# Kernel tuning notes

Measured on AMD Instinct MI355X. Metric: run time of the kernel, lower is better.

Reference implementation:

```python
import jax, jax.numpy as jnp
import numpy as np

B, T, D, DFF, H, W = 2, 2048, 1024, 4096, 16, 512
HD = D // H
EPS = 1e-6
NEG = jnp.float32(-1e30)


def _rms(x, w):
    return x * jax.lax.rsqrt(jnp.mean(x * x, axis=-1, keepdims=True) + EPS) * w


def setup_inputs() -> dict:
    key = jax.random.key(0)
    ks = jax.random.split(key, 12)
    g = lambda k, shape, std: jax.random.normal(k, shape, jnp.float32) * std
    return {
        "x": jax.random.normal(ks[0], (B, T, D), jnp.float32),
        "retrieval_context": jax.random.normal(ks[1], (B, D), jnp.float32),
        "norm1_w": jnp.ones((D,), jnp.float32),
        "qkv_w": g(ks[2], (3 * D, D), 0.02),
        "qkv_b": jnp.zeros((3 * D,), jnp.float32),
        "proj_w": g(ks[3], (D, D), 0.02),
        "proj_b": jnp.zeros((D,), jnp.float32),
        "gate_w": g(ks[4], (3, D), 0.01),
        "gate_b": jnp.zeros((3,), jnp.float32),
        "ret_w": g(ks[5], (D, D), 0.01),
        "norm2_w": jnp.ones((D,), jnp.float32),
        "ffn_gate_w": g(ks[6], (DFF, D), 0.02),
        "ffn_up_w": g(ks[7], (DFF, D), 0.02),
        "ffn_down_w": g(ks[8], (D, DFF), 0.02),
    }


def reference(x, retrieval_context, norm1_w, qkv_w, qkv_b, proj_w, proj_b,
              gate_w, gate_b, ret_w, norm2_w, ffn_gate_w, ffn_up_w, ffn_down_w):
    # pre-norm
    h = _rms(x, norm1_w)  # (B,T,D)
    # qkv projection, split into heads
    qkv = h @ qkv_w.T + qkv_b  # (B,T,3D)
    q, k, v = jnp.split(qkv, 3, axis=-1)
    to_heads = lambda t: t.reshape(B, T, H, HD).transpose(0, 2, 1, 3)  # (B,H,T,HD)
    q, k, v = to_heads(q), to_heads(k), to_heads(v)
    # sliding-window causal mask: attend to j in [i-W+1, i]
    idx = jnp.arange(T)
    win = (idx[:, None] >= idx[None, :]) & (idx[:, None] - idx[None, :] < W)  # (T,T)
    scores = jnp.einsum("bhqd,bhkd->bhqk", q, k) / np.sqrt(HD).astype(np.float32)
    scores = jnp.where(win, scores, NEG)
    attn = jax.nn.softmax(scores, axis=-1)
    attn_out = jnp.einsum("bhqk,bhkd->bhqd", attn, v)  # (B,H,T,HD)
    attn_out = attn_out.transpose(0, 2, 1, 3).reshape(B, T, D)
    attn_out = attn_out @ proj_w.T + proj_b
    # retrieval stream (TRN disabled -> zeros, gate channel 1 hard-masked)
    ret_out = (retrieval_context @ ret_w.T)[:, None, :]  # (B,1,D) broadcast over T
    gate_logits = h @ gate_w.T + gate_b  # (B,T,3)
    gate_logits = gate_logits.at[:, :, 1].set(-1e9)  # enable_trn=False
    gates = jax.nn.softmax(gate_logits, axis=-1)
    mixed = gates[:, :, 0:1] * attn_out + gates[:, :, 2:3] * ret_out
    x = x + mixed
    # SwiGLU FFN
    h2 = _rms(x, norm2_w)
    ffn = (jax.nn.silu(h2 @ ffn_gate_w.T) * (h2 @ ffn_up_w.T)) @ ffn_down_w.T
    return x + ffn
```

## Files before the change

kernel.cpp:

```cpp
#include <hip/hip_runtime.h>
#include <hip/hip_bf16.h>

typedef __bf16 bf16_t;
typedef __bf16 bf16x8 __attribute__((ext_vector_type(8)));
typedef __bf16 bf16x4v __attribute__((ext_vector_type(4)));
typedef float f32x4 __attribute__((ext_vector_type(4)));

static constexpr int Bn = 2, Tn = 2048, Dn = 1024, DFFn = 4096, Hn = 16, HDn = 64, Wn = 512;
static constexpr int Mn = Bn * Tn;

#define MFMA16(a, b, c) __builtin_amdgcn_mfma_f32_16x16x32_bf16(a, b, c, 0, 0, 0)

typedef __attribute__((address_space(3))) void lds_void;
typedef const __attribute__((address_space(1))) void gbl_void;

__global__ __launch_bounds__(256) void cvt_f32_bf16_kernel(const float4* __restrict__ src,
                                                           bf16x4v* __restrict__ dst, int n4) {
  int i = blockIdx.x * 256 + threadIdx.x;
  if (i < n4) {
    float4 v = src[i];
    bf16x4v o;
    o[0] = (bf16_t)v.x; o[1] = (bf16_t)v.y; o[2] = (bf16_t)v.z; o[3] = (bf16_t)v.w;
    dst[i] = o;
  }
}

__device__ __forceinline__ float blockReduceSum(float v, float* sbuf) {
#pragma unroll
  for (int off = 32; off > 0; off >>= 1) v += __shfl_down(v, off, 64);
  int lane = threadIdx.x & 63, wid = threadIdx.x >> 6;
  __syncthreads();
  if (lane == 0) sbuf[wid] = v;
  __syncthreads();
  return sbuf[0] + sbuf[1] + sbuf[2] + sbuf[3];
}

template <bool GATE>
__global__ __launch_bounds__(256) void rmsnorm_kernel(const float* __restrict__ x,
                                                      const float* __restrict__ w,
                                                      bf16_t* __restrict__ out,
                                                      const float* __restrict__ gw,
                                                      const float* __restrict__ gb,
                                                      float* __restrict__ gates) {
  __shared__ float sbuf[4];
  int row = blockIdx.x, tid = threadIdx.x;
  const float4* xr = (const float4*)(x + (long)row * Dn);
  float4 v = xr[tid];
  float ss = v.x * v.x + v.y * v.y + v.z * v.z + v.w * v.w;
  ss = blockReduceSum(ss, sbuf);
  float rms = rsqrtf(ss * (1.0f / Dn) + 1e-6f);
  float4 wv = ((const float4*)w)[tid];
  float h0 = v.x * rms * wv.x, h1 = v.y * rms * wv.y;
  float h2 = v.z * rms * wv.z, h3 = v.w * rms * wv.w;
  bf16x4v o;
  o[0] = (bf16_t)h0; o[1] = (bf16_t)h1; o[2] = (bf16_t)h2; o[3] = (bf16_t)h3;
  ((bf16x4v*)(out + (long)row * Dn))[tid] = o;
  if (GATE) {
    float4 g0v = ((const float4*)gw)[tid];
    float4 g2v = ((const float4*)(gw + 2 * Dn))[tid];
    float l0 = h0 * g0v.x + h1 * g0v.y + h2 * g0v.z + h3 * g0v.w;
    float l2 = h0 * g2v.x + h1 * g2v.y + h2 * g2v.z + h3 * g2v.w;
    l0 = blockReduceSum(l0, sbuf);
    l2 = blockReduceSum(l2, sbuf);
    if (tid == 0) {
      l0 += gb[0];
      l2 += gb[2];
      float mx = fmaxf(l0, l2);
      float e0 = __expf(l0 - mx), e2 = __expf(l2 - mx);
      float inv = 1.0f / (e0 + e2);
      gates[2 * row] = e0 * inv;
      gates[2 * row + 1] = e2 * inv;
    }
  }
}

__global__ __launch_bounds__(512, 2) void gemm256_kernel(const bf16_t* __restrict__ Ag,
                                                         const bf16_t* __restrict__ Wt, int K,
                                                         int N, const float* __restrict__ bias,
                                                         bf16_t* __restrict__ outb) {
  __shared__ bf16_t lds2[65536];
  const int tid = threadIdx.x;
  const int wid = tid >> 6, lane = tid & 63;
  const int wr = wid >> 2, wc = wid & 3;
  const int m0 = blockIdx.y * 256, n0 = blockIdx.x * 256;
  const int lr = lane & 15, lg = lane >> 4;
  const int lterm = (lr * 32 + lg * 8) ^ (((lr >> 3) & 1) << 4);
  const int colsw = (lane & 3) * 8 ^ (((lane >> 5) & 1) << 4);
  const int NT = K >> 6;

  auto stageA = [&](int buf, int half, int t) {
#pragma unroll
    for (int q = 0; q < 2; q++) {
      int s = q * 8 + wid, s_r = s >> 1, s_c = s & 1;
      const bf16_t* src =
          Ag + (long)(m0 + half * 128 + s_r * 16 + (lane >> 2)) * K + (long)t * 64 + s_c * 32 + colsw;
      bf16_t* dst = &lds2[buf * 32768 + (half * 8 + s_r) * 1024 + s_c * 512];
      __builtin_amdgcn_global_load_lds((gbl_void*)src, (lds_void*)dst, 16, 0, 0);
    }
  };
  auto stageB = [&](int buf, int half, int t) {
#pragma unroll
    for (int q = 0; q < 2; q++) {
      int s = q * 8 + wid, s_r = s >> 1, s_c = s & 1;
      const bf16_t* src =
          Wt + (long)(n0 + half * 128 + s_r * 16 + (lane >> 2)) * K + (long)t * 64 + s_c * 32 + colsw;
      bf16_t* dst = &lds2[buf * 32768 + 16384 + (half * 8 + s_r) * 1024 + s_c * 512];
      __builtin_amdgcn_global_load_lds((gbl_void*)src, (lds_void*)dst, 16, 0, 0);
    }
  };

  f32x4 acc[8][4];
#pragma unroll
  for (int i = 0; i < 8; i++)
#pragma unroll
    for (int j = 0; j < 4; j++) acc[i][j] = (f32x4){0.f, 0.f, 0.f, 0.f};

  stageB(0, 0, 0);
  stageB(0, 1, 0);
  stageA(0, 0, 0);
  stageA(0, 1, 0);
  if (NT > 1) {
    stageB(1, 0, 1);
    stageB(1, 1, 1);
    asm volatile("s_waitcnt vmcnt(4)" ::: "memory");
  } else {
    asm volatile("s_waitcnt vmcnt(0)" ::: "memory");
  }
  __builtin_amdgcn_sched_barrier(0);
  __builtin_amdgcn_s_barrier();

#define LDA(mi, ks) (*(const bf16x8*)&lds2[ca + ((wr << 3) + (mi)) * 1024 + (ks)*512 + lterm])
#define LDB(ni, ks) (*(const bf16x8*)&lds2[cb + ((wc << 2) + (ni)) * 1024 + (ks)*512 + lterm])

#define GPHASE(mi0, ...)                                                                  \
  do {                                                                                    \
    bf16x8 a0k0 = LDA(mi0, 0), a0k1 = LDA(mi0, 1);                                        \
    bf16x8 a1k0 = LDA((mi0) + 1, 0), a1k1 = LDA((mi0) + 1, 1);                            \
    __VA_ARGS__;                                                                          \
    __builtin_amdgcn_s_barrier();                                                         \
    asm volatile("s_waitcnt lgkmcnt(0)" ::: "memory");                                    \
    __builtin_amdgcn_sched_barrier(0);                                                    \
    __builtin_amdgcn_s_setprio(1);                                                        \
    _Pragma("unroll") for (int ni = 0; ni < 4; ni++) {                                    \
      acc[mi0][ni] = MFMA16(a0k0, bfr[ni][0], acc[mi0][ni]);                              \
      acc[mi0][ni] = MFMA16(a0k1, bfr[ni][1], acc[mi0][ni]);                              \
      acc[(mi0) + 1][ni] = MFMA16(a1k0, bfr[ni][0], acc[(mi0) + 1][ni]);                  \
      acc[(mi0) + 1][ni] = MFMA16(a1k1, bfr[ni][1], acc[(mi0) + 1][ni]);                  \
    }                                                                                     \
    __builtin_amdgcn_s_setprio(0);                                                        \
    __builtin_amdgcn_s_barrier();                                                         \
  } while (0)

#define GTILE(t, cur)                                                                     \
  do {                                                                                    \
    const int ca = (cur)*32768, cb = ca + 16384;                                          \
    bf16x8 bfr[4][2];                                                                     \
    _Pragma("unroll") for (int ni = 0; ni < 4; ni++) {                                    \
      bfr[ni][0] = LDB(ni, 0);                                                            \
      bfr[ni][1] = LDB(ni, 1);                                                            \
    }                                                                                     \
    GPHASE(0, {                                                                           \
      if ((t) + 1 < NT) {                                                                 \
        stageA(1 - (cur), 0, (t) + 1);                                                    \
        stageA(1 - (cur), 1, (t) + 1);                                                    \
      }                                                                                   \
    });                                                                                   \
    GPHASE(2, {                                                                           \
      if ((t) + 2 < NT) stageB((cur), 0, (t) + 2);                                        \
    });                                                                                   \
    GPHASE(4, {                                                                           \
      if ((t) + 2 < NT) stageB((cur), 1, (t) + 2);                                        \
    });                                                                                   \
    GPHASE(6, {});                                                                        \
    if ((t) + 1 < NT) {                                                                   \
      if ((t) + 2 < NT)                                                                   \
        asm volatile("s_waitcnt vmcnt(4)" ::: "memory");                                  \
      else                                                                                \
        asm volatile("s_waitcnt vmcnt(0)" ::: "memory");                                  \
      __builtin_amdgcn_sched_barrier(0);                                                  \
      __builtin_amdgcn_s_barrier();                                                       \
    }                                                                                     \
  } while (0)

  for (int t = 0; t < NT; t += 2) {
    GTILE(t, 0);
    GTILE(t + 1, 1);
  }

#pragma unroll
  for (int mi = 0; mi < 8; mi++) {
#pragma unroll
    for (int rr = 0; rr < 4; rr++) {
      long r = m0 + wr * 128 + mi * 16 + lg * 4 + rr;
#pragma unroll
      for (int ni = 0; ni < 4; ni++) {
        int c = n0 + wc * 64 + ni * 16 + lr;
        float v = acc[mi][ni][rr];
        if (bias) v += bias[c];
        outb[r * N + c] = (bf16_t)v;
      }
    }
  }
#undef LDA
#undef LDB
#undef GPHASE
#undef GTILE
}

template <int EPI>
__global__ __launch_bounds__(256) void gemm_kernel(const bf16_t* __restrict__ A,
                                                   const bf16_t* __restrict__ Wt, int K, int N,
                                                   const float* __restrict__ bias,
                                                   bf16_t* __restrict__ outb,
                                                   float* __restrict__ outf,
                                                   const float* __restrict__ gates,
                                                   const float* __restrict__ ret,
                                                   const float* __restrict__ resid) {
  __shared__ bf16_t smem[8192];
  const int tid = threadIdx.x;
  const int w = tid >> 6, lane = tid & 63;
  const int wr = w >> 1, wc = w & 1;
  const int m0 = blockIdx.y * 128, n0 = blockIdx.x * 128;

  const bf16_t* gsrc[4];
#pragma unroll
  for (int q = 0; q < 4; q++) {
    int e = ((w * 4 + q) * 64 + lane) * 8;
    int rr = (e & 4095) >> 5, cc = e & 31;
    gsrc[q] = (e < 4096) ? (A + (long)(m0 + rr) * K + cc) : (Wt + (long)(n0 + rr) * K + cc);
  }
  bf16_t* lbase = &smem[(w * 4) * 512];

  f32x4 acc[4][4];
#pragma unroll
  for (int i = 0; i < 4; i++)
#pragma unroll
    for (int j = 0; j < 4; j++) acc[i][j] = (f32x4){0.f, 0.f, 0.f, 0.f};

  const int lr = lane & 15, lc = (lane >> 4) * 8;

  for (int kt = 0; kt < K; kt += 32) {
    if (kt) __syncthreads();
#pragma unroll
    for (int q = 0; q < 4; q++) {
      __builtin_amdgcn_global_load_lds((gbl_void*)(gsrc[q] + kt), (lds_void*)(lbase + q * 512), 16,
                                       0, 0);
    }
    __syncthreads();

    bf16x8 af[4], bfv[4];
#pragma unroll
    for (int i = 0; i < 4; i++) af[i] = *(const bf16x8*)&smem[(wr * 64 + i * 16 + lr) * 32 + lc];
#pragma unroll
    for (int i = 0; i < 4; i++)
      bfv[i] = *(const bf16x8*)&smem[4096 + (wc * 64 + i * 16 + lr) * 32 + lc];
#pragma unroll
    for (int mi = 0; mi < 4; mi++)
#pragma unroll
      for (int ni = 0; ni < 4; ni++) acc[mi][ni] = MFMA16(af[mi], bfv[ni], acc[mi][ni]);
  }

  const int lrow4 = (lane >> 4) * 4;
#pragma unroll
  for (int mi = 0; mi < 4; mi++) {
#pragma unroll
    for (int rr2 = 0; rr2 < 4; rr2++) {
      int r = m0 + wr * 64 + mi * 16 + lrow4 + rr2;
      float g0 = 0.f, g2 = 0.f;
      const float* retb = nullptr;
      if (EPI == 2) {
        g0 = gates[2 * r];
        g2 = gates[2 * r + 1];
        retb = ret + ((r >> 11) << 10);
      }
#pragma unroll
      for (int ni = 0; ni < 4; ni++) {
        int c = n0 + wc * 64 + ni * 16 + (lane & 15);
        float v = acc[mi][ni][rr2];
        long idx = (long)r * N + c;
        if (EPI == 0) {
          if (bias) v += bias[c];
          outb[idx] = (bf16_t)v;
        } else if (EPI == 2) {
          outf[idx] = resid[idx] + g0 * (v + bias[c]) + g2 * retb[c];
        } else {
          outf[idx] = resid[idx] + v;
        }
      }
    }
  }
}

__global__ __launch_bounds__(256) void retproj_kernel(const float* __restrict__ rc,
                                                      const float* __restrict__ rw,
                                                      float* __restrict__ out) {
  int gw = blockIdx.x * 4 + (threadIdx.x >> 6);
  int lane = threadIdx.x & 63;
  int b = gw >> 10, n = gw & 1023;
  float v = 0.f;
  for (int k = lane; k < Dn; k += 64) v += rc[b * Dn + k] * rw[(long)n * Dn + k];
#pragma unroll
  for (int off = 32; off > 0; off >>= 1) v += __shfl_down(v, off, 64);
  if (lane == 0) out[gw] = v;
}

__global__ __launch_bounds__(256) void attn_kernel(const bf16_t* __restrict__ qkv,
                                                   bf16_t* __restrict__ out) {
  __shared__ bf16_t psh[4][512];
  const int tid = threadIdx.x, w = tid >> 6, lane = tid & 63;
  const int qb = blockIdx.x, bh = blockIdx.y;
  const int b = bh >> 4, h = bh & 15;
  const int qw0 = qb * 64 + w * 16;
  const bf16_t* base = qkv + (long)b * Tn * 3072 + h * 64;
  const bf16_t* kb = base + Dn;
  const bf16_t* vb = base + 2 * Dn;
  const int lr = lane & 15, lg = lane >> 4;

  bf16x8 aq0 = *(const bf16x8*)(base + (long)(qw0 + lr) * 3072 + lg * 8);
  bf16x8 aq1 = *(const bf16x8*)(base + (long)(qw0 + lr) * 3072 + lg * 8 + 32);

  float m_run[4], l_run[4];
  f32x4 accv[4];
#pragma unroll
  for (int r = 0; r < 4; r++) { m_run[r] = -1e30f; l_run[r] = 0.f; }
#pragma unroll
  for (int c = 0; c < 4; c++) accv[c] = (f32x4){0.f, 0.f, 0.f, 0.f};

  int j_lo = qw0 - (Wn - 1);
  if (j_lo < 0) j_lo = 0;
  j_lo &= ~31;
  const int j_hi = qw0 + 15;

  for (int j0 = j_lo; j0 <= j_hi; j0 += 32) {
    f32x4 s[2];
#pragma unroll
    for (int hh = 0; hh < 2; hh++) {
      const bf16_t* kr = kb + (long)(j0 + hh * 16 + lr) * 3072 + lg * 8;
      bf16x8 k0 = *(const bf16x8*)kr;
      bf16x8 k1 = *(const bf16x8*)(kr + 32);
      f32x4 z = (f32x4){0.f, 0.f, 0.f, 0.f};
      z = MFMA16(aq0, k0, z);
      z = MFMA16(aq1, k1, z);
      s[hh] = z;
    }
    float mt[4];
#pragma unroll
    for (int r = 0; r < 4; r++) {
      int q = qw0 + lg * 4 + r;
      int c0 = j0 + lr, c1 = j0 + 16 + lr;
      float s0 = (q >= c0 && (q - c0) < Wn) ? s[0][r] * 0.125f : -1e30f;
      float s1 = (q >= c1 && (q - c1) < Wn) ? s[1][r] * 0.125f : -1e30f;
      s[0][r] = s0;
      s[1][r] = s1;
      mt[r] = fmaxf(s0, s1);
    }
#pragma unroll
    for (int off = 1; off < 16; off <<= 1)
#pragma unroll
      for (int r = 0; r < 4; r++) mt[r] = fmaxf(mt[r], __shfl_xor(mt[r], off, 64));
    float rs[4];
#pragma unroll
    for (int r = 0; r < 4; r++) {
      float nm = fmaxf(m_run[r], mt[r]);
      float alpha = __expf(m_run[r] - nm);
      m_run[r] = nm;
      float p0 = __expf(s[0][r] - nm);
      float p1 = __expf(s[1][r] - nm);
      psh[w][(lg * 4 + r) * 32 + lr] = (bf16_t)p0;
      psh[w][(lg * 4 + r) * 32 + 16 + lr] = (bf16_t)p1;
      rs[r] = p0 + p1;
      l_run[r] *= alpha;
#pragma unroll
      for (int c = 0; c < 4; c++) accv[c][r] *= alpha;
    }
#pragma unroll
    for (int off = 1; off < 16; off <<= 1)
#pragma unroll
      for (int r = 0; r < 4; r++) rs[r] += __shfl_xor(rs[r], off, 64);
#pragma unroll
    for (int r = 0; r < 4; r++) l_run[r] += rs[r];

    bf16x8 ap = *(const bf16x8*)&psh[w][lr * 32 + lg * 8];
#pragma unroll
    for (int c = 0; c < 4; c++) {
      bf16x8 bv;
#pragma unroll
      for (int jj = 0; jj < 8; jj++) bv[jj] = vb[(long)(j0 + lg * 8 + jj) * 3072 + c * 16 + lr];
      accv[c] = MFMA16(ap, bv, accv[c]);
    }
  }
#pragma unroll
  for (int r = 0; r < 4; r++) {
    float inv = 1.0f / l_run[r];
    long orow = ((long)b * Tn + qw0 + lg * 4 + r) * Dn + h * 64;
#pragma unroll
    for (int c = 0; c < 4; c++) out[orow + c * 16 + lr] = (bf16_t)(accv[c][r] * inv);
  }
}

__global__ __launch_bounds__(256) void silu_mul_kernel(const bf16_t* __restrict__ gu,
                                                       bf16_t* __restrict__ act) {
  int m = blockIdx.y;
  int j0 = (blockIdx.x * 256 + threadIdx.x) * 8;
  bf16x8 g = *(const bf16x8*)(gu + (long)m * (2 * DFFn) + j0);
  bf16x8 u = *(const bf16x8*)(gu + (long)m * (2 * DFFn) + DFFn + j0);
  bf16x8 o;
#pragma unroll
  for (int i = 0; i < 8; i++) {
    float gf = (float)g[i], uf = (float)u[i];
    float sf = gf / (1.0f + __expf(-gf));
    o[i] = (bf16_t)(sf * uf);
  }
  *(bf16x8*)(act + (long)m * DFFn + j0) = o;
}

extern "C" void kernel_launch(void* const* d_in, const int* in_sizes, int n_in, void* d_out,
                              int out_size, void* d_ws, size_t ws_size, hipStream_t stream) {
  const float* x = (const float*)d_in[0];
  const float* rc = (const float*)d_in[1];
  const float* n1w = (const float*)d_in[2];
  const float* qkv_w = (const float*)d_in[3];
  const float* qkv_b = (const float*)d_in[4];
  const float* proj_w = (const float*)d_in[5];
  const float* proj_b = (const float*)d_in[6];
  const float* gate_w = (const float*)d_in[7];
  const float* gate_b = (const float*)d_in[8];
  const float* ret_w = (const float*)d_in[9];
  const float* n2w = (const float*)d_in[10];
  const float* fgw = (const float*)d_in[11];
  const float* fuw = (const float*)d_in[12];
  const float* fdw = (const float*)d_in[13];
  float* out = (float*)d_out;

  char* ws = (char*)d_ws;
  size_t off = 0;
  auto alloc = [&](size_t bytes) {
    char* p = ws + off;
    off += (bytes + 255) & ~(size_t)255;
    return p;
  };
  bf16_t* wqkv = (bf16_t*)alloc(3072l * 1024 * 2);
  bf16_t* wproj = (bf16_t*)alloc(1024l * 1024 * 2);
  bf16_t* wgup = (bf16_t*)alloc(8192l * 1024 * 2);
  bf16_t* wdown = (bf16_t*)alloc(1024l * 4096 * 2);
  bf16_t* h1 = (bf16_t*)alloc((long)Mn * 1024 * 2);
  bf16_t* h2 = (bf16_t*)alloc((long)Mn * 1024 * 2);
  bf16_t* qkvb = (bf16_t*)alloc((long)Mn * 3072 * 2);
  bf16_t* attnb = (bf16_t*)alloc((long)Mn * 1024 * 2);
  bf16_t* gupo = (bf16_t*)alloc((long)Mn * 8192 * 2);
  bf16_t* actb = (bf16_t*)alloc((long)Mn * 4096 * 2);
  float* gates = (float*)alloc((long)Mn * 2 * 4);
  float* retb = (float*)alloc(2048 * 4);
  float* xmid = (float*)alloc((long)Mn * 1024 * 4);

  cvt_f32_bf16_kernel<<<3072, 256, 0, stream>>>((const float4*)qkv_w, (bf16x4v*)wqkv, 786432);
  cvt_f32_bf16_kernel<<<1024, 256, 0, stream>>>((const float4*)proj_w, (bf16x4v*)wproj, 262144);
  cvt_f32_bf16_kernel<<<4096, 256, 0, stream>>>((const float4*)fgw, (bf16x4v*)wgup, 1048576);
  cvt_f32_bf16_kernel<<<4096, 256, 0, stream>>>((const float4*)fuw, (bf16x4v*)(wgup + 4194304),
                                                1048576);
  cvt_f32_bf16_kernel<<<4096, 256, 0, stream>>>((const float4*)fdw, (bf16x4v*)wdown, 1048576);

  rmsnorm_kernel<true><<<Mn, 256, 0, stream>>>(x, n1w, h1, gate_w, gate_b, gates);
  gemm256_kernel<<<dim3(12, 16), 512, 0, stream>>>(h1, wqkv, 1024, 3072, qkv_b, qkvb);
  retproj_kernel<<<512, 256, 0, stream>>>(rc, ret_w, retb);
  attn_kernel<<<dim3(32, 32), 256, 0, stream>>>(qkvb, attnb);
  gemm_kernel<2><<<dim3(8, 32), 256, 0, stream>>>(attnb, wproj, 1024, 1024, proj_b, nullptr, xmid,
                                                  gates, retb, x);
  rmsnorm_kernel<false><<<Mn, 256, 0, stream>>>(xmid, n2w, h2, nullptr, nullptr, nullptr);
  gemm256_kernel<<<dim3(32, 16), 512, 0, stream>>>(h2, wgup, 1024, 8192, nullptr, gupo);
  silu_mul_kernel<<<dim3(2, 4096), 256, 0, stream>>>(gupo, actb);
  gemm_kernel<3><<<dim3(8, 32), 256, 0, stream>>>(actb, wdown, 4096, 1024, nullptr, nullptr, out,
                                                  nullptr, nullptr, xmid);
}
```

Before: 486.5 us.

## Double-buffer 128x128 GEMM with BK=64 and swizzled LDS layout

Rewrites the 128x128 GEMM used for the attention-output projection and the FFN down projection. It now stages 64-wide K tiles into two LDS buffers, so the next tile's global-to-LDS load overlaps the current tile's MFMAs, and it uses one barrier per tile instead of two. Loads go into an XOR-swizzled 16x32 sub-tile layout to cut LDS bank conflicts. LDS use grows from 16KB to 64KB per block, which may lower occupancy.

```diff
diff --git a/kernel.cpp b/kernel.cpp
--- a/kernel.cpp
+++ b/kernel.cpp
@@ -208,28 +208,36 @@
 }
 
 template <int EPI>
-__global__ __launch_bounds__(256) void gemm_kernel(const bf16_t* __restrict__ A,
-                                                   const bf16_t* __restrict__ Wt, int K, int N,
-                                                   const float* __restrict__ bias,
-                                                   bf16_t* __restrict__ outb,
-                                                   float* __restrict__ outf,
-                                                   const float* __restrict__ gates,
-                                                   const float* __restrict__ ret,
-                                                   const float* __restrict__ resid) {
-  __shared__ bf16_t smem[8192];
-  const int tid = threadIdx.x;
-  const int w = tid >> 6, lane = tid & 63;
-  const int wr = w >> 1, wc = w & 1;
+__global__ __launch_bounds__(256) void gemm128_kernel(const bf16_t* __restrict__ A,
+                                                      const bf16_t* __restrict__ Wt, int K, int N,
+                                                      const float* __restrict__ bias,
+                                                      float* __restrict__ outf,
+                                                      const float* __restrict__ gates,
+                                                      const float* __restrict__ ret,
+                                                      const float* __restrict__ resid) {
+  __shared__ bf16_t lds[32768];
+  const int tid = threadIdx.x, wid = tid >> 6, lane = tid & 63;
+  const int wr = wid >> 1, wc = wid & 1;
   const int m0 = blockIdx.y * 128, n0 = blockIdx.x * 128;
-
-  const bf16_t* gsrc[4];
-#pragma unroll
-  for (int q = 0; q < 4; q++) {
-    int e = ((w * 4 + q) * 64 + lane) * 8;
-    int rr = (e & 4095) >> 5, cc = e & 31;
-    gsrc[q] = (e < 4096) ? (A + (long)(m0 + rr) * K + cc) : (Wt + (long)(n0 + rr) * K + cc);
-  }
-  bf16_t* lbase = &smem[(w * 4) * 512];
+  const int lr = lane & 15, lg = lane >> 4;
+  const int lterm = (lr * 32 + lg * 8) ^ (((lr >> 3) & 1) << 4);
+  const int colsw = (lane & 3) * 8 ^ (((lane >> 5) & 1) << 4);
+  const int NT = K >> 6;
+
+  auto stage = [&](int buf, int t) {
+#pragma unroll
+    for (int q = 0; q < 8; q++) {
+      int c = wid * 8 + q;
+      int isB = c >> 4;
+      int cc = c & 15;
+      int s_r = cc >> 1, s_c = cc & 1;
+      const bf16_t* base = isB ? Wt + (long)(n0 + s_r * 16 + (lane >> 2)) * K
+                               : A + (long)(m0 + s_r * 16 + (lane >> 2)) * K;
+      const bf16_t* src = base + (long)t * 64 + s_c * 32 + colsw;
+      bf16_t* dst = &lds[buf * 16384 + isB * 8192 + (s_r * 2 + s_c) * 512];
+      __builtin_amdgcn_global_load_lds((gbl_void*)src, (lds_void*)dst, 16, 0, 0);
+    }
+  };
 
   f32x4 acc[4][4];
 #pragma unroll
@@ -237,35 +245,35 @@
 #pragma unroll
     for (int j = 0; j < 4; j++) acc[i][j] = (f32x4){0.f, 0.f, 0.f, 0.f};
 
-  const int lr = lane & 15, lc = (lane >> 4) * 8;
-
-  for (int kt = 0; kt < K; kt += 32) {
-    if (kt) __syncthreads();
-#pragma unroll
-    for (int q = 0; q < 4; q++) {
-      __builtin_amdgcn_global_load_lds((gbl_void*)(gsrc[q] + kt), (lds_void*)(lbase + q * 512), 16,
-                                       0, 0);
-    }
-    __syncthreads();
-
-    bf16x8 af[4], bfv[4];
-#pragma unroll
-    for (int i = 0; i < 4; i++) af[i] = *(const bf16x8*)&smem[(wr * 64 + i * 16 + lr) * 32 + lc];
-#pragma unroll
-    for (int i = 0; i < 4; i++)
-      bfv[i] = *(const bf16x8*)&smem[4096 + (wc * 64 + i * 16 + lr) * 32 + lc];
-#pragma unroll
-    for (int mi = 0; mi < 4; mi++)
-#pragma unroll
-      for (int ni = 0; ni < 4; ni++) acc[mi][ni] = MFMA16(af[mi], bfv[ni], acc[mi][ni]);
-  }
-
-  const int lrow4 = (lane >> 4) * 4;
+  stage(0, 0);
+  __syncthreads();
+
+  for (int t = 0; t < NT; t++) {
+    const int cur = t & 1;
+    if (t + 1 < NT) stage(cur ^ 1, t + 1);
+    const int ab = cur * 16384;
+#pragma unroll
+    for (int ks = 0; ks < 2; ks++) {
+      bf16x8 af[4], bfv[4];
+#pragma unroll
+      for (int mi = 0; mi < 4; mi++)
+        af[mi] = *(const bf16x8*)&lds[ab + ((wr * 4 + mi) * 2 + ks) * 512 + lterm];
+#pragma unroll
+      for (int ni = 0; ni < 4; ni++)
+        bfv[ni] = *(const bf16x8*)&lds[ab + 8192 + ((wc * 4 + ni) * 2 + ks) * 512 + lterm];
+#pragma unroll
+      for (int mi = 0; mi < 4; mi++)
+#pragma unroll
+        for (int ni = 0; ni < 4; ni++) acc[mi][ni] = MFMA16(af[mi], bfv[ni], acc[mi][ni]);
+    }
+    if (t + 1 < NT) __syncthreads();
+  }
+
 #pragma unroll
   for (int mi = 0; mi < 4; mi++) {
 #pragma unroll
     for (int rr2 = 0; rr2 < 4; rr2++) {
-      int r = m0 + wr * 64 + mi * 16 + lrow4 + rr2;
+      int r = m0 + wr * 64 + mi * 16 + lg * 4 + rr2;
       float g0 = 0.f, g2 = 0.f;
       const float* retb = nullptr;
       if (EPI == 2) {
@@ -275,13 +283,10 @@
       }
 #pragma unroll
       for (int ni = 0; ni < 4; ni++) {
-        int c = n0 + wc * 64 + ni * 16 + (lane & 15);
+        int c = n0 + wc * 64 + ni * 16 + lr;
         float v = acc[mi][ni][rr2];
         long idx = (long)r * N + c;
-        if (EPI == 0) {
-          if (bias) v += bias[c];
-          outb[idx] = (bf16_t)v;
-        } else if (EPI == 2) {
+        if (EPI == 2) {
           outf[idx] = resid[idx] + g0 * (v + bias[c]) + g2 * retb[c];
         } else {
           outf[idx] = resid[idx] + v;
@@ -464,11 +469,11 @@
   gemm256_kernel<<<dim3(12, 16), 512, 0, stream>>>(h1, wqkv, 1024, 3072, qkv_b, qkvb);
   retproj_kernel<<<512, 256, 0, stream>>>(rc, ret_w, retb);
   attn_kernel<<<dim3(32, 32), 256, 0, stream>>>(qkvb, attnb);
-  gemm_kernel<2><<<dim3(8, 32), 256, 0, stream>>>(attnb, wproj, 1024, 1024, proj_b, nullptr, xmid,
-                                                  gates, retb, x);
+  gemm128_kernel<2><<<dim3(8, 32), 256, 0, stream>>>(attnb, wproj, 1024, 1024, proj_b, xmid, gates,
+                                                     retb, x);
   rmsnorm_kernel<false><<<Mn, 256, 0, stream>>>(xmid, n2w, h2, nullptr, nullptr, nullptr);
   gemm256_kernel<<<dim3(32, 16), 512, 0, stream>>>(h2, wgup, 1024, 8192, nullptr, gupo);
   silu_mul_kernel<<<dim3(2, 4096), 256, 0, stream>>>(gupo, actb);
-  gemm_kernel<3><<<dim3(8, 32), 256, 0, stream>>>(actb, wdown, 4096, 1024, nullptr, nullptr, out,
-                                                  nullptr, nullptr, xmid);
-}
+  gemm128_kernel<3><<<dim3(8, 32), 256, 0, stream>>>(actb, wdown, 4096, 1024, nullptr, out,
+                                                     nullptr, nullptr, xmid);
+}
```

New measurement: 431.5 us. -11.3%, faster.
